# Kernel optimization log

Measured on AMD Instinct MI355X. Metric: run time of the kernel, lower is better.

The kernel has to match this reference:

```python
import jax, jax.numpy as jnp
import numpy as np
from jax import lax

# Static configuration (matches init_kwargs / input_specs)
B, DIM, H, W = 4, 192, 64, 64
HEADS, SR, WS = 8, 4, 3
HD = DIM // HEADS            # 24
LL = WS * WS                 # 9  (local window length)
N = H * W                    # 4096 tokens
PH, PW = H // SR, W // SR    # 16, 16 pooled grid
PLEN = PH * PW               # 256
PRETRAIN = 512 // 8          # img_size // 2**(i+2) with i=1 -> 64


def _ln(x, g, b, eps=1e-5):
    m = x.mean(-1, keepdims=True)
    v = ((x - m) ** 2).mean(-1, keepdims=True)
    return (x - m) / jnp.sqrt(v + eps) * g + b


def _l2norm(x):
    n = jnp.sqrt(jnp.sum(x * x, -1, keepdims=True))
    return x / jnp.maximum(n, 1e-12)


def _build_static():
    # get_relative_position_cpb: adaptive 1d pool of arange gives key coords
    qh = np.arange(H, dtype=np.float64)
    qw = np.arange(W, dtype=np.float64)
    kh = qh.reshape(PH, SR).mean(-1)  # H divisible by SR -> uniform bins
    kw = qw.reshape(PW, SR).mean(-1)
    KH, KW = np.meshgrid(kh, kw, indexing='ij')
    QH, QW = np.meshgrid(qh, qw, indexing='ij')
    rel_h = (QH.reshape(-1)[:, None] - KH.reshape(-1)[None, :]) / (PRETRAIN - 1) * 8
    rel_w = (QW.reshape(-1)[:, None] - KW.reshape(-1)[None, :]) / (PRETRAIN - 1) * 8
    rel_hw = np.stack([rel_h, rel_w], -1).reshape(-1, 2)
    table, idx = np.unique(rel_hw, axis=0, return_inverse=True)
    table = np.sign(table) * np.log2(np.abs(table) + 1.0) / np.log2(8.0)
    # get_seqlen_and_mask: validity of each of the 9 neighbors per position
    hh, ww = np.meshgrid(np.arange(H), np.arange(W), indexing='ij')
    hh, ww = hh.reshape(-1), ww.reshape(-1)
    valid = np.stack([(hh + dh >= 0) & (hh + dh < H) & (ww + dw >= 0) & (ww + dw < W)
                      for dh in (-1, 0, 1) for dw in (-1, 0, 1)], -1)  # [N, 9]
    pad_mask = ~valid
    seq_scale = np.log(valid.sum(-1, keepdims=True).astype(np.float64) + PLEN).astype(np.float32)  # [N,1]
    return idx.reshape(-1).astype(np.int32), table.astype(np.float32), seq_scale, pad_mask


def setup_inputs() -> dict:
    key = jax.random.key(0)
    ks = jax.random.split(key, 12)
    f32 = jnp.float32

    def tn(k, shape, std=0.02):
        return jax.random.truncated_normal(k, -2.0, 2.0, shape, f32) * std

    rel_idx, table, seq_scale, pad_mask = _build_static()
    return dict(
        x=jax.random.normal(ks[0], (B, DIM, H, W), f32),
        pe_w=tn(ks[1], (DIM, DIM, 3, 3)),
        pe_b=jnp.zeros((DIM,), f32),
        pe_ln_g=jnp.ones((DIM,), f32), pe_ln_b=jnp.zeros((DIM,), f32),
        q_w=tn(ks[2], (DIM, DIM)), q_b=jnp.zeros((DIM,), f32),
        kv_w=tn(ks[3], (2 * DIM, DIM)), kv_b=jnp.zeros((2 * DIM,), f32),
        sr_w=tn(ks[4], (DIM, DIM)), sr_b=jnp.zeros((DIM,), f32),
        norm_g=jnp.ones((DIM,), f32), norm_b=jnp.zeros((DIM,), f32),
        cpb1_w=tn(ks[5], (512, 2), 0.1), cpb1_b=jnp.zeros((512,), f32),
        cpb2_w=tn(ks[6], (HEADS, 512), 0.05), cpb2_b=jnp.zeros((HEADS,), f32),
        rpb_local=tn(ks[7], (HEADS, LL), 0.0004),
        learnable_tokens=tn(ks[8], (HEADS, HD, LL)),
        learnable_bias=jnp.zeros((HEADS, 1, LL), f32),
        query_embedding=tn(ks[9], (HEADS, 1, HD)),
        temperature=jnp.full((HEADS, 1, 1), float(np.log(np.exp(1.0 / 0.24) - 1.0)), f32),
        proj_w=tn(ks[10], (DIM, DIM)), proj_b=jnp.zeros((DIM,), f32),
        out_ln_g=jnp.ones((DIM,), f32), out_ln_b=jnp.zeros((DIM,), f32),
        rel_idx=jnp.asarray(rel_idx),
        coords_table=jnp.asarray(table),
        seq_scale=jnp.asarray(seq_scale),
        pad_mask=jnp.asarray(pad_mask),
    )


def _forward(x, pe_w, pe_b, pe_ln_g, pe_ln_b, q_w, q_b, kv_w, kv_b, sr_w, sr_b,
             norm_g, norm_b, cpb1_w, cpb1_b, cpb2_w, cpb2_b, rpb_local,
             learnable_tokens, learnable_bias, query_embedding, temperature,
             proj_w, proj_b, out_ln_g, out_ln_b,
             rel_idx, coords_table, seq_scale, pad_mask):
    # OverlapPatchEmbed: 3x3 conv s1 p1 -> tokens -> LN
    xc = lax.conv_general_dilated(x, pe_w, (1, 1), ((1, 1), (1, 1)),
                                  dimension_numbers=('NCHW', 'OIHW', 'NCHW')) + pe_b[None, :, None, None]
    t = _ln(xc.reshape(B, DIM, N).transpose(0, 2, 1), pe_ln_g, pe_ln_b)  # [B,N,C]

    # queries
    q = t @ q_w.T + q_b
    q_norm = _l2norm(q.reshape(B, N, HEADS, HD).transpose(0, 2, 1, 3))   # [B,h,N,d]
    q_scaled = (q_norm + query_embedding[None]) * jax.nn.softplus(temperature)[None] * seq_scale

    # local KV via 3x3 neighborhood gather (torch nn.Unfold)
    kv = t @ kv_w.T + kv_b                                               # [B,N,2C]
    k_loc = _l2norm(kv[..., :DIM].reshape(B, N, HEADS, HD)).reshape(B, N, DIM)
    kv_map = jnp.concatenate([k_loc, kv[..., DIM:]], -1).transpose(0, 2, 1).reshape(B, 2 * DIM, H, W)
    p = jnp.pad(kv_map, ((0, 0), (0, 0), (1, 1), (1, 1)))
    neigh = jnp.stack([p[:, :, kh:kh + H, kw:kw + W] for kh in range(WS) for kw in range(WS)], 2)
    neigh = neigh.reshape(B, 2 * HEADS, HD, LL, N).transpose(0, 1, 4, 2, 3)  # [B,2h,N,d,9]
    k_local, v_local = neigh[:, :HEADS], neigh[:, HEADS:]
    attn_local = jnp.einsum('bhnd,bhndl->bhnl', q_scaled, k_local) + rpb_local[None, :, None, :]
    attn_local = jnp.where(pad_mask[None, None], -jnp.inf, attn_local)   # [B,h,N,9]

    # pooled global KV: 1x1 conv -> GELU -> adaptive avg pool -> LN -> kv
    x_map = t.transpose(0, 2, 1).reshape(B, DIM, H, W)
    sr_out = jax.nn.gelu(jnp.einsum('oc,bchw->bohw', sr_w, x_map) + sr_b[None, :, None, None],
                         approximate=False)
    pooled = sr_out.reshape(B, DIM, PH, SR, PW, SR).mean((3, 5)).reshape(B, DIM, PLEN).transpose(0, 2, 1)
    pooled = _ln(pooled, norm_g, norm_b)
    kv_p = (pooled @ kv_w.T + kv_b).reshape(B, PLEN, 2 * HEADS, HD).transpose(0, 2, 1, 3)
    k_pool, v_pool = kv_p[:, :HEADS], kv_p[:, HEADS:]

    # CPB relative position bias for the pooled branch
    cpb = jax.nn.relu(coords_table @ cpb1_w.T + cpb1_b) @ cpb2_w.T + cpb2_b  # [T,h]
    pool_bias = cpb.T[:, rel_idx].reshape(HEADS, N, PLEN)
    attn_pool = jnp.einsum('bhnd,bhmd->bhnm', q_scaled, _l2norm(k_pool)) + pool_bias[None]

    # joint softmax over local + pooled keys
    attn = jax.nn.softmax(jnp.concatenate([attn_local, attn_pool], -1), -1)
    a_loc, a_pool = attn[..., :LL], attn[..., LL:]

    w_loc = jnp.einsum('bhnd,hdl->bhnl', q_norm, learnable_tokens) + learnable_bias[None] + a_loc
    x_local = jnp.einsum('bhnl,bhndl->bhnd', w_loc, v_local)
    x_pool = jnp.einsum('bhnm,bhmd->bhnd', a_pool, v_pool)

    out = (x_local + x_pool).transpose(0, 2, 1, 3).reshape(B, N, DIM) @ proj_w.T + proj_b
    out = _ln(out, out_ln_g, out_ln_b)
    return out.transpose(0, 2, 1).reshape(B, DIM, H, W)


def reference(x, pe_w, pe_b, pe_ln_g, pe_ln_b, q_w, q_b, kv_w, kv_b, sr_w, sr_b,
              norm_g, norm_b, cpb1_w, cpb1_b, cpb2_w, cpb2_b, rpb_local,
              learnable_tokens, learnable_bias, query_embedding, temperature,
              proj_w, proj_b, out_ln_g, out_ln_b,
              rel_idx, coords_table, seq_scale, pad_mask):
    return _forward(x, pe_w, pe_b, pe_ln_g, pe_ln_b, q_w, q_b, kv_w, kv_b, sr_w, sr_b,
                    norm_g, norm_b, cpb1_w, cpb1_b, cpb2_w, cpb2_b, rpb_local,
                    learnable_tokens, learnable_bias, query_embedding, temperature,
                    proj_w, proj_b, out_ln_g, out_ln_b,
                    rel_idx, coords_table, seq_scale, pad_mask)
```

## Files before the change

kernel.cpp:

```cpp
#include <hip/hip_runtime.h>
#include <stdint.h>


__device__ __forceinline__ float b2f(unsigned short u) {
  return __uint_as_float(((unsigned)u) << 16);
}
__device__ __forceinline__ unsigned short f2b(float f) {
  unsigned x = __float_as_uint(f);
  return (unsigned short)((x + 0x7fffu + ((x >> 16) & 1u)) >> 16);
}

constexpr size_t OFF_T    = 0;
constexpr size_t OFF_KMAP = 3145728;
constexpr size_t OFF_QN   = 9437184;
constexpr size_t OFF_QS   = 12582912;
constexpr size_t OFF_CTX  = 15728640;
constexpr size_t OFF_POOL = 18874368;
constexpr size_t OFF_KP   = 19070976;
constexpr size_t OFF_VP   = 19267584;
constexpr size_t OFF_CPB  = 19464192;
constexpr size_t OFF_BIAS = 19595264;
constexpr size_t OFF_WTC  = OFF_CTX;
constexpr size_t OFF_QT   = OFF_CTX + 331776;
constexpr size_t OFF_KVT  = OFF_CTX + 368640;
constexpr size_t OFF_SRT  = OFF_CTX + 442368;
constexpr size_t OFF_PJT  = OFF_KMAP;

__global__ __launch_bounds__(256) void k_wt_conv(const float* __restrict__ pw,
                                                 float* __restrict__ wt) {
  int i = blockIdx.x * 256 + threadIdx.x;
  if (i >= 331776) return;
  int oc = i % 192, k = i / 192;
  wt[i] = pw[(size_t)oc * 1728 + k];
}
__global__ __launch_bounds__(256) void k_wt_gen(const float* __restrict__ src,
                                                float* __restrict__ dst, int O, int K) {
  int i = blockIdx.x * 256 + threadIdx.x;
  if (i >= O * K) return;
  int o = i % O, k = i / O;
  dst[i] = src[(size_t)o * K + k];
}

__global__ __launch_bounds__(256) void k_conv(
    const float* __restrict__ x, const float* __restrict__ wtc,
    float* __restrict__ t0, float* __restrict__ t1, float* __restrict__ t2) {
  __shared__ float xl[8 * 4 * 66];
  const int tid = threadIdx.x;
  const int lane = tid & 63;
  const int wv = __builtin_amdgcn_readfirstlane(tid >> 6);
  const int h0 = blockIdx.x * 2;
  const int b = blockIdx.y;
  const int zz = blockIdx.z;
  const int obase = (zz & 3) * 48;
  const int ith = zz >> 2;
  const int icb = ith * 8;
  const int ow = obase + wv * 12;

  float acc0[12], acc1[12];
#pragma unroll
  for (int j = 0; j < 12; ++j) { acc0[j] = 0.f; acc1[j] = 0.f; }

  float xr[9];
  auto loadx = [&](int ic0) {
#pragma unroll
    for (int s = 0; s < 9; ++s) {
      int f = tid + s * 256;
      float v = 0.f;
      if (f < 2112) {
        int ii = f / 264;
        int rem = f - ii * 264;
        int r = rem / 66;
        int wp = rem - r * 66;
        int hh = h0 + r - 1, ww = wp - 1;
        if (hh >= 0 && hh < 64 && ww >= 0 && ww < 64)
          v = x[((size_t)(b * 192 + ic0 * 8 + ii) << 12) + (hh << 6) + ww];
      }
      xr[s] = v;
    }
  };
  loadx(icb);

  for (int i2 = 0; i2 < 8; ++i2) {
    const int ic0 = icb + i2;
    __syncthreads();
#pragma unroll
    for (int s = 0; s < 9; ++s) {
      int f = tid + s * 256;
      if (f < 2112) {
        int ii = f / 264;
        int rem = f - ii * 264;
        int r = rem / 66;
        int wp = rem - r * 66;
        xl[(ii * 4 + r) * 66 + wp] = xr[s];
      }
    }
    __syncthreads();
    if (i2 < 7) loadx(ic0 + 1);
    const float* wb = wtc + (size_t)ic0 * 72 * 192 + ow;
#pragma unroll 1
    for (int ii = 0; ii < 8; ++ii) {
      float xv[4][3];
#pragma unroll
      for (int r4 = 0; r4 < 4; ++r4) {
        const float* xp = &xl[(ii * 4 + r4) * 66 + lane];
        xv[r4][0] = xp[0]; xv[r4][1] = xp[1]; xv[r4][2] = xp[2];
      }
#pragma unroll
      for (int r = 0; r < 3; ++r) {
#pragma unroll
        for (int kw = 0; kw < 3; ++kw) {
          const float4* wp = (const float4*)(wb + (size_t)(ii * 9 + r * 3 + kw) * 192);
          float4 wA = wp[0], wB = wp[1], wC = wp[2];
          float xv0 = xv[r][kw], xv1 = xv[r + 1][kw];
          acc0[0]  += xv0 * wA.x;  acc1[0]  += xv1 * wA.x;
          acc0[1]  += xv0 * wA.y;  acc1[1]  += xv1 * wA.y;
          acc0[2]  += xv0 * wA.z;  acc1[2]  += xv1 * wA.z;
          acc0[3]  += xv0 * wA.w;  acc1[3]  += xv1 * wA.w;
          acc0[4]  += xv0 * wB.x;  acc1[4]  += xv1 * wB.x;
          acc0[5]  += xv0 * wB.y;  acc1[5]  += xv1 * wB.y;
          acc0[6]  += xv0 * wB.z;  acc1[6]  += xv1 * wB.z;
          acc0[7]  += xv0 * wB.w;  acc1[7]  += xv1 * wB.w;
          acc0[8]  += xv0 * wC.x;  acc1[8]  += xv1 * wC.x;
          acc0[9]  += xv0 * wC.y;  acc1[9]  += xv1 * wC.y;
          acc0[10] += xv0 * wC.z;  acc1[10] += xv1 * wC.z;
          acc0[11] += xv0 * wC.w;  acc1[11] += xv1 * wC.w;
        }
      }
    }
  }
  float* tdst = (ith == 0) ? t0 : ((ith == 1) ? t1 : t2);
  float* out0 = tdst + ((size_t)b * 4096 + h0 * 64 + lane) * 192 + ow;
  float* out1 = out0 + 64 * 192;
#pragma unroll
  for (int j4 = 0; j4 < 3; ++j4) {
    float4 v0, v1;
    v0.x = acc0[j4 * 4 + 0];  v1.x = acc1[j4 * 4 + 0];
    v0.y = acc0[j4 * 4 + 1];  v1.y = acc1[j4 * 4 + 1];
    v0.z = acc0[j4 * 4 + 2];  v1.z = acc1[j4 * 4 + 2];
    v0.w = acc0[j4 * 4 + 3];  v1.w = acc1[j4 * 4 + 3];
    ((float4*)out0)[j4] = v0;
    ((float4*)out1)[j4] = v1;
  }
}

__global__ __launch_bounds__(256) void k_ln_rows(float* __restrict__ data,
    const float* __restrict__ data2, const float* __restrict__ data3,
    const float* __restrict__ cbias,
    const float* __restrict__ g, const float* __restrict__ be, int rows) {
  int lane = threadIdx.x & 63;
  int wv = threadIdx.x >> 6;
  int row = blockIdx.x * 4 + wv;
  if (row >= rows) return;
  float* p = data + (size_t)row * 192;
  float v0 = p[lane], v1 = p[lane + 64], v2 = p[lane + 128];
  if (data2) {
    const float* p2 = data2 + (size_t)row * 192;
    v0 += p2[lane]; v1 += p2[lane + 64]; v2 += p2[lane + 128];
  }
  if (data3) {
    const float* p3 = data3 + (size_t)row * 192;
    v0 += p3[lane]; v1 += p3[lane + 64]; v2 += p3[lane + 128];
  }
  if (cbias) {
    v0 += cbias[lane]; v1 += cbias[lane + 64]; v2 += cbias[lane + 128];
  }
  float s = v0 + v1 + v2;
  float sq = v0 * v0 + v1 * v1 + v2 * v2;
#pragma unroll
  for (int m = 32; m >= 1; m >>= 1) {
    s += __shfl_xor(s, m, 64);
    sq += __shfl_xor(sq, m, 64);
  }
  float mean = s * (1.f / 192.f);
  float var = sq * (1.f / 192.f) - mean * mean;
  float rstd = rsqrtf(var + 1e-5f);
  p[lane]       = (v0 - mean) * rstd * g[lane]       + be[lane];
  p[lane + 64]  = (v1 - mean) * rstd * g[lane + 64]  + be[lane + 64];
  p[lane + 128] = (v2 - mean) * rstd * g[lane + 128] + be[lane + 128];
}

template <int OCB, typename GXV, typename GXD>
__device__ __forceinline__ void gemm_tiles(
    float* __restrict__ wl, float* __restrict__ xs, int tid, int lane, int wv,
    const float* __restrict__ wt, int ostr, int obase,
    float (&acc)[OCB / 4], GXV gxv, GXD gxd) {
  constexpr int NPF4 = OCB / 4;
  constexpr int NW4 = OCB / 16;
  constexpr int NWR = (32 * NPF4 + 255) / 256;
  constexpr bool WEXACT = (32 * NPF4 % 256) == 0;
  float xr[8];
  float4 wr[NWR];
  auto loadx = [&](int k0) {
#pragma unroll
    for (int s = 0; s < 8; ++s) xr[s] = gxv(k0, tid + s * 256);
  };
  auto loadw = [&](int k0) {
#pragma unroll
    for (int s = 0; s < NWR; ++s) {
      int f4 = tid + s * 256;
      if (WEXACT || f4 < 32 * NPF4) {
        int kk = f4 / NPF4, j = f4 - kk * NPF4;
        wr[s] = ((const float4*)(wt + (size_t)(k0 + kk) * ostr + obase))[j];
      }
    }
  };
  loadx(0); loadw(0);
  for (int kt = 0; kt < 6; ++kt) {
    __syncthreads();
#pragma unroll
    for (int s = 0; s < 8; ++s) xs[gxd(tid + s * 256)] = xr[s];
#pragma unroll
    for (int s = 0; s < NWR; ++s) {
      int f4 = tid + s * 256;
      if (WEXACT || f4 < 32 * NPF4) ((float4*)wl)[f4] = wr[s];
    }
    __syncthreads();
    if (kt < 5) { loadx((kt + 1) * 32); loadw((kt + 1) * 32); }
#pragma unroll 4
    for (int kk = 0; kk < 32; ++kk) {
      float xv = xs[kk * 66 + lane];
      const float4* wrow = (const float4*)&wl[kk * OCB + wv * NW4 * 4];
#pragma unroll
      for (int j4 = 0; j4 < NW4; ++j4) {
        float4 w4 = wrow[j4];
        acc[j4 * 4 + 0] += xv * w4.x;
        acc[j4 * 4 + 1] += xv * w4.y;
        acc[j4 * 4 + 2] += xv * w4.z;
        acc[j4 * 4 + 3] += xv * w4.w;
      }
    }
  }
}

__global__ __launch_bounds__(256) void k_q(
    const float* __restrict__ t, const float* __restrict__ qt, const float* __restrict__ qb,
    const float* __restrict__ qe, const float* __restrict__ tmp, const float* __restrict__ ss,
    float* __restrict__ qno, float* __restrict__ qso) {
  __shared__ __align__(16) float wl[32 * 96];
  __shared__ float xs[32 * 66];
  const int tid = threadIdx.x;
  const int lane = tid & 63;
  const int wv = __builtin_amdgcn_readfirstlane(tid >> 6);
  const int n0 = blockIdx.x * 64;
  const int b = blockIdx.y;
  const int obase = blockIdx.z * 96;
  const int hh = blockIdx.z * 4 + wv;
  const int oc0 = obase + wv * 24;
  float acc[24];
#pragma unroll
  for (int j = 0; j < 24; ++j) acc[j] = 0.f;

  gemm_tiles<96>(wl, xs, tid, lane, wv, qt, 192, obase, acc,
    [&](int k0, int f) {
      int nl = f >> 5, kk = f & 31;
      return t[((size_t)b * 4096 + n0 + nl) * 192 + k0 + kk];
    },
    [&](int f) { return (f & 31) * 66 + (f >> 5); });

  const int n = n0 + lane;
  float ssv = ss[n];
  float sumsq = 0.f;
#pragma unroll
  for (int d = 0; d < 24; ++d) {
    float v = acc[d] + qb[oc0 + d];
    sumsq += v * v;
  }
  float rn = 1.f / fmaxf(sqrtf(sumsq), 1e-12f);
  float sp = log1pf(__expf(tmp[hh]));
#pragma unroll
  for (int d = 0; d < 24; ++d) {
    float qv = (acc[d] + qb[oc0 + d]) * rn;
    size_t o = ((size_t)(b * 8 + hh) * 24 + d) * 4096 + n;
    qno[o] = qv;
    qso[o] = (qv + qe[hh * 24 + d]) * sp * ssv;
  }
}

__global__ __launch_bounds__(256) void k_kv(
    const float* __restrict__ t, const float* __restrict__ kvt, const float* __restrict__ kb_,
    float* __restrict__ kmap) {
  __shared__ __align__(16) float wl[32 * 96];
  __shared__ float xs[32 * 66];
  const int tid = threadIdx.x;
  const int lane = tid & 63;
  const int wv = __builtin_amdgcn_readfirstlane(tid >> 6);
  const int n0 = blockIdx.x * 64;
  const int b = blockIdx.y;
  const int obase = blockIdx.z * 96;
  const int oc0 = obase + wv * 24;
  const int n = n0 + lane;
  float acc[24];
#pragma unroll
  for (int j = 0; j < 24; ++j) acc[j] = 0.f;

  gemm_tiles<96>(wl, xs, tid, lane, wv, kvt, 384, obase, acc,
    [&](int k0, int f) {
      int nl = f >> 5, kk = f & 31;
      return t[((size_t)b * 4096 + n0 + nl) * 192 + k0 + kk];
    },
    [&](int f) { return (f & 31) * 66 + (f >> 5); });

  if (oc0 < 192) {
    float sumsq = 0.f;
#pragma unroll
    for (int d = 0; d < 24; ++d) {
      float v = acc[d] + kb_[oc0 + d];
      sumsq += v * v;
    }
    float rn = 1.f / fmaxf(sqrtf(sumsq), 1e-12f);
#pragma unroll
    for (int d = 0; d < 24; ++d)
      kmap[((size_t)b * 384 + oc0 + d) * 4096 + n] = (acc[d] + kb_[oc0 + d]) * rn;
  } else {
#pragma unroll
    for (int d = 0; d < 24; ++d)
      kmap[((size_t)b * 384 + oc0 + d) * 4096 + n] = acc[d] + kb_[oc0 + d];
  }
}

__device__ __forceinline__ float gelu_exact(float v) {
  float u = v * 0.70710678118654752f;
  float a = fabsf(u);
  float tt = 1.f / (1.f + 0.3275911f * a);
  float poly = ((((1.061405429f * tt - 1.453152027f) * tt + 1.421413741f) * tt
                 - 0.284496736f) * tt + 0.254829592f) * tt;
  float erfa = 1.f - poly * __expf(-a * a);
  float erfv = (u < 0.f) ? -erfa : erfa;
  return 0.5f * v * (1.f + erfv);
}

__global__ __launch_bounds__(256) void k_srpool(
    const float* __restrict__ t, const float* __restrict__ srt, const float* __restrict__ sb,
    float* __restrict__ pooled) {
  __shared__ __align__(16) float wl[32 * 48];
  __shared__ float xs[32 * 66];
  const int tid = threadIdx.x;
  const int lane = tid & 63;
  const int wv = __builtin_amdgcn_readfirstlane(tid >> 6);
  const int wx = blockIdx.x & 3;
  const int obase = (blockIdx.x >> 2) * 48;
  const int ph = blockIdx.y;
  const int b = blockIdx.z;
  const int oc0 = obase + wv * 12;
  float acc[12];
#pragma unroll
  for (int j = 0; j < 12; ++j) acc[j] = 0.f;

  gemm_tiles<48>(wl, xs, tid, lane, wv, srt, 192, obase, acc,
    [&](int k0, int f) {
      int pl = f >> 5, kk = f & 31;
      int row = (ph * 4 + (pl >> 4)) * 64 + wx * 16 + (pl & 15);
      return t[((size_t)b * 4096 + row) * 192 + k0 + kk];
    },
    [&](int f) { return (f & 31) * 66 + (f >> 5); });

#pragma unroll
  for (int j = 0; j < 12; ++j) {
    float gv = gelu_exact(acc[j] + sb[oc0 + j]);
    gv += __shfl_xor(gv, 1, 64);
    gv += __shfl_xor(gv, 2, 64);
    gv += __shfl_xor(gv, 16, 64);
    gv += __shfl_xor(gv, 32, 64);
    if ((lane & 51) == 0) {
      int cell = (lane >> 2) & 3;
      int p = ph * 16 + wx * 4 + cell;
      pooled[((size_t)b * 256 + p) * 192 + oc0 + j] = gv * (1.f / 16.f);
    }
  }
}

__global__ __launch_bounds__(256) void k_kvp(
    const float* __restrict__ pooled, const float* __restrict__ kvt, const float* __restrict__ kb_,
    float* __restrict__ kp, float* __restrict__ vp) {
  __shared__ __align__(16) float wl[32 * 96];
  __shared__ float xs[32 * 66];
  const int tid = threadIdx.x;
  const int lane = tid & 63;
  const int wv = __builtin_amdgcn_readfirstlane(tid >> 6);
  const int r0 = blockIdx.x * 64;
  const int obase = blockIdx.y * 96;
  const int oc0 = obase + wv * 24;
  const int row = r0 + lane;
  const int b = row >> 8;
  const int m = row & 255;
  float acc[24];
#pragma unroll
  for (int j = 0; j < 24; ++j) acc[j] = 0.f;

  gemm_tiles<96>(wl, xs, tid, lane, wv, kvt, 384, obase, acc,
    [&](int k0, int f) {
      int nl = f >> 5, kk = f & 31;
      return pooled[(size_t)(r0 + nl) * 192 + k0 + kk];
    },
    [&](int f) { return (f & 31) * 66 + (f >> 5); });

  if (oc0 < 192) {
    int hh = oc0 / 24;
    float sumsq = 0.f;
#pragma unroll
    for (int d = 0; d < 24; ++d) {
      float v = acc[d] + kb_[oc0 + d];
      sumsq += v * v;
    }
    float rn = 1.f / fmaxf(sqrtf(sumsq), 1e-12f);
#pragma unroll
    for (int d = 0; d < 24; ++d)
      kp[(((size_t)(b * 8 + hh)) * 256 + m) * 24 + d] = (acc[d] + kb_[oc0 + d]) * rn;
  } else {
    int hh = (oc0 - 192) / 24;
#pragma unroll
    for (int d = 0; d < 24; ++d)
      vp[(((size_t)(b * 8 + hh)) * 256 + m) * 24 + d] = acc[d] + kb_[oc0 + d];
  }
}

__global__ __launch_bounds__(256) void k_cpb(
    const float* __restrict__ coords, const float* __restrict__ c1w,
    const float* __restrict__ c1b, const float* __restrict__ c2w,
    const float* __restrict__ c2b, float* __restrict__ cpb, int T) {
  __shared__ float s1w[1024];
  __shared__ float s1b[512];
  __shared__ __align__(16) float s2w[512 * 8];
  const int tid = threadIdx.x;
  for (int f = tid; f < 1024; f += 256) s1w[f] = c1w[f];
  for (int f = tid; f < 512; f += 256) s1b[f] = c1b[f];
  for (int f = tid; f < 4096; f += 256) {
    int h = f >> 9, j = f & 511;
    s2w[j * 8 + h] = c2w[f];
  }
  __syncthreads();
  int i = blockIdx.x * 256 + tid;
  int ic = (i < T) ? i : (T - 1);
  float x0 = coords[2 * ic], y0 = coords[2 * ic + 1];
  float a[8];
#pragma unroll
  for (int h = 0; h < 8; ++h) a[h] = c2b[h];
#pragma unroll 4
  for (int j = 0; j < 512; ++j) {
    float hv = fmaxf(s1w[2 * j] * x0 + s1w[2 * j + 1] * y0 + s1b[j], 0.f);
    const float4* w2 = (const float4*)&s2w[j * 8];
    float4 wA = w2[0], wB = w2[1];
    a[0] += hv * wA.x; a[1] += hv * wA.y; a[2] += hv * wA.z; a[3] += hv * wA.w;
    a[4] += hv * wB.x; a[5] += hv * wB.y; a[6] += hv * wB.z; a[7] += hv * wB.w;
  }
  if (i < T) {
#pragma unroll
    for (int h = 0; h < 8; ++h) cpb[(size_t)i * 8 + h] = a[h];
  }
}

__global__ __launch_bounds__(256) void k_bias(
    const int* __restrict__ rel, const float* __restrict__ cpb,
    unsigned short* __restrict__ bt) {
  int g = blockIdx.x * 256 + threadIdx.x;
  int n = g >> 5;
  int m0 = (g & 31) * 8;
  const int4* r4 = (const int4*)(rel + (size_t)n * 256 + m0);
  int4 ra = r4[0], rb = r4[1];
  int idxs[8] = {ra.x, ra.y, ra.z, ra.w, rb.x, rb.y, rb.z, rb.w};
  unsigned acc[8][4];
#pragma unroll
  for (int j = 0; j < 8; ++j) {
    const float4* c4 = (const float4*)(cpb + (size_t)idxs[j] * 8);
    float4 A = c4[0], Bv = c4[1];
    float vals[8] = {A.x, A.y, A.z, A.w, Bv.x, Bv.y, Bv.z, Bv.w};
#pragma unroll
    for (int hh = 0; hh < 8; ++hh) {
      unsigned u = f2b(vals[hh]);
      if (j & 1) acc[hh][j >> 1] |= u << 16;
      else       acc[hh][j >> 1]  = u;
    }
  }
#pragma unroll
  for (int hh = 0; hh < 8; ++hh) {
    uint4 o;
    o.x = acc[hh][0]; o.y = acc[hh][1]; o.z = acc[hh][2]; o.w = acc[hh][3];
    *(uint4*)(bt + ((size_t)hh * 4096 + n) * 256 + m0) = o;
  }
}

__global__ __launch_bounds__(512, 4) void k_attn(
    const float* __restrict__ qs_g, const float* __restrict__ qn_g,
    const float* __restrict__ kmap, const float* __restrict__ kp, const float* __restrict__ vp,
    const unsigned short* __restrict__ bt, const float* __restrict__ rpb,
    const float* __restrict__ lt, const float* __restrict__ lb,
    float* __restrict__ ctx) {
  __shared__ __align__(16) float smem[12288];
  float* kl = smem;
  float* vl = smem + 6144;
  const int tid = threadIdx.x;
  const int lane = tid & 63;
  const int w = __builtin_amdgcn_readfirstlane(tid >> 6);
  const int qm = w & 3;
  const int rr = w >> 2;
  const int row = blockIdx.x * 2 + rr;
  const int h = blockIdx.y;
  const int b = blockIdx.z;
  const int n = (row << 6) + lane;
  const float SHIFT = 15.f;

  {
    const float4* kps = (const float4*)(kp + (size_t)(b * 8 + h) * 6144);
    const float4* vps = (const float4*)(vp + (size_t)(b * 8 + h) * 6144);
    float4* kld = (float4*)kl;
    float4* vld = (float4*)vl;
#pragma unroll
    for (int c = 0; c < 3; ++c) {
      int f = tid + c * 512;
      kld[f] = kps[f];
      vld[f] = vps[f];
    }
  }

  float qsv[24];
  {
    const float* qsb = qs_g + ((size_t)(b * 8 + h) * 24) * 4096 + n;
#pragma unroll
    for (int d = 0; d < 24; ++d) qsv[d] = qsb[(size_t)d * 4096];
  }

  const int l0 = (qm == 1) ? 0 : ((qm == 0) ? 3 : (qm * 2 + 1));
  const int lcnt = (qm == 1) ? 3 : 2;

  float wlv[3];
  {
    float qnv[24];
    const float* qnb = qn_g + ((size_t)(b * 8 + h) * 24) * 4096 + n;
#pragma unroll
    for (int d = 0; d < 24; ++d) qnv[d] = qnb[(size_t)d * 4096];
    const float* ltp = lt + h * 216;
    const float* lbp = lb + h * 9;
#pragma unroll
    for (int j = 0; j < 3; ++j) {
      float a = 0.f;
      if (j < lcnt) {
        int l = l0 + j;
#pragma unroll
        for (int d = 0; d < 24; ++d) a += qnv[d] * ltp[d * 9 + l];
        a += lbp[l];
      }
      wlv[j] = a;
    }
  }

  float ctxA[24], ctxBP[24];
#pragma unroll
  for (int d = 0; d < 24; ++d) { ctxA[d] = 0.f; ctxBP[d] = 0.f; }
  float S = 0.f;

  {
    const float* kbase = kmap + ((size_t)b * 384 + h * 24) * 4096;
    const float* rpp = rpb + h * 9;
    for (int j = 0; j < lcnt; ++j) {
      const int l = l0 + j;
      const int dh = l / 3 - 1, dw = l % 3 - 1;
      const int hp = row + dh;
      if (hp < 0 || hp >= 64) continue;
      const int wp2 = lane + dw;
      const bool okw = (wp2 >= 0) && (wp2 < 64);
      const int nn = (hp << 6) + (okw ? wp2 : lane);
      const float* kb = kbase + nn;
      const float* vb = kb + (size_t)192 * 4096;
      float d0 = 0, d1 = 0, d2 = 0, d3 = 0;
#pragma unroll
      for (int d = 0; d < 24; d += 4) {
        d0 += qsv[d] * kb[(size_t)d * 4096];
        d1 += qsv[d + 1] * kb[(size_t)(d + 1) * 4096];
        d2 += qsv[d + 2] * kb[(size_t)(d + 2) * 4096];
        d3 += qsv[d + 3] * kb[(size_t)(d + 3) * 4096];
      }
      float p = okw ? __expf((d0 + d1) + (d2 + d3) + rpp[l] - SHIFT) : 0.f;
      S += p;
      float wll = okw ? wlv[j] : 0.f;
#pragma unroll
      for (int d = 0; d < 24; ++d) {
        float vv = vb[(size_t)d * 4096];
        ctxA[d] += wll * vv;
        ctxBP[d] += p * vv;
      }
    }
  }

  __syncthreads();

  {
    const unsigned short* bp = bt + ((size_t)h * 4096 + n) * 256 + qm * 64;
    const float* klq = kl + qm * (64 * 24);
    const float* vlq = vl + qm * (64 * 24);
    uint4 bcur = *(const uint4*)bp;
#pragma unroll 1
    for (int c = 0; c < 8; ++c) {
      uint4 bnx = bcur;
      if (c < 7) bnx = *(const uint4*)(bp + (c + 1) * 8);
#pragma unroll
      for (int j = 0; j < 8; ++j) {
        const float4* kr4 = (const float4*)&klq[(c * 8 + j) * 24];
        const float4* vr4 = (const float4*)&vlq[(c * 8 + j) * 24];
        float d0 = 0, d1 = 0, d2 = 0, d3 = 0;
#pragma unroll
        for (int q4 = 0; q4 < 6; ++q4) {
          float4 k4 = kr4[q4];
          d0 += qsv[q4 * 4 + 0] * k4.x;
          d1 += qsv[q4 * 4 + 1] * k4.y;
          d2 += qsv[q4 * 4 + 2] * k4.z;
          d3 += qsv[q4 * 4 + 3] * k4.w;
        }
        unsigned word = (j < 2) ? bcur.x : (j < 4) ? bcur.y : (j < 6) ? bcur.z : bcur.w;
        float bv = (j & 1) ? __uint_as_float(word & 0xffff0000u)
                           : __uint_as_float(word << 16);
        float p = __expf((d0 + d1) + (d2 + d3) + bv - SHIFT);
        S += p;
#pragma unroll
        for (int q4 = 0; q4 < 6; ++q4) {
          float4 v4 = vr4[q4];
          ctxBP[q4 * 4 + 0] += p * v4.x;
          ctxBP[q4 * 4 + 1] += p * v4.y;
          ctxBP[q4 * 4 + 2] += p * v4.z;
          ctxBP[q4 * 4 + 3] += p * v4.w;
        }
      }
      bcur = bnx;
    }
  }

  for (int src = 1; src < 4; ++src) {
    __syncthreads();
    if (qm == src) {
      float* p = smem + (size_t)(rr * 64 + lane) * 49;
      p[0] = S;
#pragma unroll
      for (int d = 0; d < 24; ++d) { p[1 + d] = ctxA[d]; p[25 + d] = ctxBP[d]; }
    }
    __syncthreads();
    if (qm == 0) {
      const float* p = smem + (size_t)(rr * 64 + lane) * 49;
      S += p[0];
#pragma unroll
      for (int d = 0; d < 24; ++d) { ctxA[d] += p[1 + d]; ctxBP[d] += p[25 + d]; }
    }
  }
  if (qm == 0) {
    const float inv = 1.f / S;
    float* cb = ctx + ((size_t)(b * 8 + h) * 24) * 4096 + n;
#pragma unroll
    for (int d = 0; d < 24; ++d)
      cb[(size_t)d * 4096] = ctxA[d] + ctxBP[d] * inv;
  }
}

__global__ __launch_bounds__(256) void k_projg(
    const float* __restrict__ ctx, const float* __restrict__ pjt, const float* __restrict__ pb,
    float* __restrict__ pout) {
  __shared__ __align__(16) float wl[32 * 96];
  __shared__ float xs[32 * 66];
  const int tid = threadIdx.x;
  const int lane = tid & 63;
  const int wv = __builtin_amdgcn_readfirstlane(tid >> 6);
  const int n0 = blockIdx.x * 64;
  const int b = blockIdx.y;
  const int obase = blockIdx.z * 96;
  const int oc0 = obase + wv * 24;
  const int n = n0 + lane;
  float acc[24];
#pragma unroll
  for (int j = 0; j < 24; ++j) acc[j] = 0.f;

  gemm_tiles<96>(wl, xs, tid, lane, wv, pjt, 192, obase, acc,
    [&](int k0, int f) {
      int kk = f >> 6, nl = f & 63;
      return ctx[((size_t)b * 192 + k0 + kk) * 4096 + n0 + nl];
    },
    [&](int f) { return (f >> 6) * 66 + (f & 63); });

#pragma unroll
  for (int d = 0; d < 24; ++d)
    pout[((size_t)b * 192 + oc0 + d) * 4096 + n] = acc[d] + pb[oc0 + d];
}

__global__ __launch_bounds__(256) void k_oln(
    const float* __restrict__ pout, const float* __restrict__ g,
    const float* __restrict__ be, float* __restrict__ out) {
  __shared__ float red[2][4][64];
  const int tid = threadIdx.x;
  const int lane = tid & 63;
  const int wv = __builtin_amdgcn_readfirstlane(tid >> 6);
  const int n0 = blockIdx.x * 64;
  const int b = blockIdx.y;
  const int o0 = wv * 48;
  float v[48];
  float s = 0.f, sq = 0.f;
#pragma unroll
  for (int j = 0; j < 48; ++j) {
    v[j] = pout[((size_t)b * 192 + o0 + j) * 4096 + n0 + lane];
    s += v[j];
    sq += v[j] * v[j];
  }
  red[0][wv][lane] = s;
  red[1][wv][lane] = sq;
  __syncthreads();
  float st = red[0][0][lane] + red[0][1][lane] + red[0][2][lane] + red[0][3][lane];
  float sqt = red[1][0][lane] + red[1][1][lane] + red[1][2][lane] + red[1][3][lane];
  float mean = st * (1.f / 192.f);
  float var = sqt * (1.f / 192.f) - mean * mean;
  float rstd = rsqrtf(var + 1e-5f);
#pragma unroll
  for (int j = 0; j < 48; ++j) {
    int o = o0 + j;
    out[((size_t)b * 192 + o) * 4096 + n0 + lane] = (v[j] - mean) * rstd * g[o] + be[o];
  }
}

extern "C" void kernel_launch(void* const* d_in, const int* in_sizes, int n_in,
                              void* d_out, int out_size, void* d_ws, size_t ws_size,
                              hipStream_t stream) {
  float* w = (float*)d_ws;

  const float* x      = (const float*)d_in[0];
  const float* pe_w   = (const float*)d_in[1];
  const float* pe_b   = (const float*)d_in[2];
  const float* peln_g = (const float*)d_in[3];
  const float* peln_b = (const float*)d_in[4];
  const float* q_w    = (const float*)d_in[5];
  const float* q_b    = (const float*)d_in[6];
  const float* kv_w   = (const float*)d_in[7];
  const float* kv_b   = (const float*)d_in[8];
  const float* sr_w   = (const float*)d_in[9];
  const float* sr_b   = (const float*)d_in[10];
  const float* norm_g = (const float*)d_in[11];
  const float* norm_b = (const float*)d_in[12];
  const float* cpb1w  = (const float*)d_in[13];
  const float* cpb1b  = (const float*)d_in[14];
  const float* cpb2w  = (const float*)d_in[15];
  const float* cpb2b  = (const float*)d_in[16];
  const float* rpb    = (const float*)d_in[17];
  const float* lt     = (const float*)d_in[18];
  const float* lb     = (const float*)d_in[19];
  const float* qe     = (const float*)d_in[20];
  const float* temp   = (const float*)d_in[21];
  const float* proj_w = (const float*)d_in[22];
  const float* proj_b = (const float*)d_in[23];
  const float* oln_g  = (const float*)d_in[24];
  const float* oln_b  = (const float*)d_in[25];
  const int*   rel    = (const int*)d_in[26];
  const float* coords = (const float*)d_in[27];
  const float* ss     = (const float*)d_in[28];

  dim3 blk(256);
  k_wt_conv<<<dim3(1296), blk, 0, stream>>>(pe_w, w + OFF_WTC);
  k_wt_gen<<<dim3(144), blk, 0, stream>>>(q_w, w + OFF_QT, 192, 192);
  k_wt_gen<<<dim3(288), blk, 0, stream>>>(kv_w, w + OFF_KVT, 384, 192);
  k_wt_gen<<<dim3(144), blk, 0, stream>>>(sr_w, w + OFF_SRT, 192, 192);

  k_conv<<<dim3(32, 4, 12), blk, 0, stream>>>(x, w + OFF_WTC, w + OFF_T,
      w + OFF_KMAP, w + OFF_KMAP + 3145728);
  k_ln_rows<<<dim3(4096), blk, 0, stream>>>(w + OFF_T, w + OFF_KMAP,
      w + OFF_KMAP + 3145728, pe_b, peln_g, peln_b, 16384);
  k_q<<<dim3(64, 4, 2), blk, 0, stream>>>(w + OFF_T, w + OFF_QT, q_b, qe, temp, ss,
      w + OFF_QN, w + OFF_QS);
  k_kv<<<dim3(64, 4, 4), blk, 0, stream>>>(w + OFF_T, w + OFF_KVT, kv_b, w + OFF_KMAP);
  k_srpool<<<dim3(16, 16, 4), blk, 0, stream>>>(w + OFF_T, w + OFF_SRT, sr_b, w + OFF_POOL);
  k_ln_rows<<<dim3(256), blk, 0, stream>>>(w + OFF_POOL, nullptr, nullptr, nullptr,
      norm_g, norm_b, 1024);
  k_kvp<<<dim3(16, 4), blk, 0, stream>>>(w + OFF_POOL, w + OFF_KVT, kv_b,
      w + OFF_KP, w + OFF_VP);
  int T = in_sizes[27] / 2;
  k_cpb<<<dim3((T + 255) / 256), blk, 0, stream>>>(coords, cpb1w, cpb1b, cpb2w, cpb2b,
      w + OFF_CPB, T);
  k_bias<<<dim3(512), blk, 0, stream>>>(rel, w + OFF_CPB,
      (unsigned short*)(w + OFF_BIAS));
  k_attn<<<dim3(32, 8, 4), dim3(512), 0, stream>>>(w + OFF_QS, w + OFF_QN, w + OFF_KMAP,
      w + OFF_KP, w + OFF_VP, (const unsigned short*)(w + OFF_BIAS), rpb, lt, lb,
      w + OFF_CTX);
  k_wt_gen<<<dim3(144), blk, 0, stream>>>(proj_w, w + OFF_PJT, 192, 192);
  k_projg<<<dim3(64, 4, 2), blk, 0, stream>>>(w + OFF_CTX, w + OFF_PJT, proj_b,
      w + OFF_QN);
  k_oln<<<dim3(64, 4), blk, 0, stream>>>(w + OFF_QN, oln_g, oln_b, (float*)d_out);
}
```

Baseline: 608.2 us.

## Compute four output rows per conv block and split input channels six ways

Each block of the 3x3 patch-embed convolution now computes four output rows instead of two, so every weight float4 fetched is reused across four rows. To keep the same block count, the input-channel reduction is split into six partial sums instead of three. The extra partial buffers borrow the QN, QS and BIAS workspace regions, and the row LayerNorm kernel now adds up to six partial inputs. The cost is more partial-sum memory traffic, more accumulator registers, and a possible overrun if the BIAS region is smaller than one full partial buffer.

Measured after the change: 606.5 us. About the same (-0.3%).

```diff
diff --git a/kernel.cpp b/kernel.cpp
--- a/kernel.cpp
+++ b/kernel.cpp
@@ -43,32 +43,35 @@
 
 __global__ __launch_bounds__(256) void k_conv(
     const float* __restrict__ x, const float* __restrict__ wtc,
-    float* __restrict__ t0, float* __restrict__ t1, float* __restrict__ t2) {
-  __shared__ float xl[8 * 4 * 66];
+    float* __restrict__ p0, float* __restrict__ p1, float* __restrict__ p2,
+    float* __restrict__ p3, float* __restrict__ p4, float* __restrict__ p5) {
+  __shared__ float xl[8 * 6 * 66];
   const int tid = threadIdx.x;
   const int lane = tid & 63;
   const int wv = __builtin_amdgcn_readfirstlane(tid >> 6);
-  const int h0 = blockIdx.x * 2;
+  const int h0 = blockIdx.x * 4;
   const int b = blockIdx.y;
   const int zz = blockIdx.z;
   const int obase = (zz & 3) * 48;
   const int ith = zz >> 2;
-  const int icb = ith * 8;
+  const int icb = ith * 4;
   const int ow = obase + wv * 12;
 
-  float acc0[12], acc1[12];
-#pragma unroll
-  for (int j = 0; j < 12; ++j) { acc0[j] = 0.f; acc1[j] = 0.f; }
-
-  float xr[9];
+  float acc[4][12];
+#pragma unroll
+  for (int ro = 0; ro < 4; ++ro)
+#pragma unroll
+    for (int j = 0; j < 12; ++j) acc[ro][j] = 0.f;
+
+  float xr[13];
   auto loadx = [&](int ic0) {
 #pragma unroll
-    for (int s = 0; s < 9; ++s) {
+    for (int s = 0; s < 13; ++s) {
       int f = tid + s * 256;
       float v = 0.f;
-      if (f < 2112) {
-        int ii = f / 264;
-        int rem = f - ii * 264;
+      if (f < 3168) {
+        int ii = f / 396;
+        int rem = f - ii * 396;
         int r = rem / 66;
         int wp = rem - r * 66;
         int hh = h0 + r - 1, ww = wp - 1;
@@ -80,72 +83,78 @@
   };
   loadx(icb);
 
-  for (int i2 = 0; i2 < 8; ++i2) {
+  for (int i2 = 0; i2 < 4; ++i2) {
     const int ic0 = icb + i2;
     __syncthreads();
 #pragma unroll
-    for (int s = 0; s < 9; ++s) {
+    for (int s = 0; s < 13; ++s) {
       int f = tid + s * 256;
-      if (f < 2112) {
-        int ii = f / 264;
-        int rem = f - ii * 264;
+      if (f < 3168) {
+        int ii = f / 396;
+        int rem = f - ii * 396;
         int r = rem / 66;
         int wp = rem - r * 66;
-        xl[(ii * 4 + r) * 66 + wp] = xr[s];
+        xl[(ii * 6 + r) * 66 + wp] = xr[s];
       }
     }
     __syncthreads();
-    if (i2 < 7) loadx(ic0 + 1);
+    if (i2 < 3) loadx(ic0 + 1);
     const float* wb = wtc + (size_t)ic0 * 72 * 192 + ow;
 #pragma unroll 1
     for (int ii = 0; ii < 8; ++ii) {
-      float xv[4][3];
-#pragma unroll
-      for (int r4 = 0; r4 < 4; ++r4) {
-        const float* xp = &xl[(ii * 4 + r4) * 66 + lane];
-        xv[r4][0] = xp[0]; xv[r4][1] = xp[1]; xv[r4][2] = xp[2];
-      }
-#pragma unroll
-      for (int r = 0; r < 3; ++r) {
+      float xv[6][3];
+#pragma unroll
+      for (int r6 = 0; r6 < 6; ++r6) {
+        const float* xp = &xl[(ii * 6 + r6) * 66 + lane];
+        xv[r6][0] = xp[0]; xv[r6][1] = xp[1]; xv[r6][2] = xp[2];
+      }
+#pragma unroll
+      for (int kh = 0; kh < 3; ++kh) {
 #pragma unroll
         for (int kw = 0; kw < 3; ++kw) {
-          const float4* wp = (const float4*)(wb + (size_t)(ii * 9 + r * 3 + kw) * 192);
+          const float4* wp = (const float4*)(wb + (size_t)(ii * 9 + kh * 3 + kw) * 192);
           float4 wA = wp[0], wB = wp[1], wC = wp[2];
-          float xv0 = xv[r][kw], xv1 = xv[r + 1][kw];
-          acc0[0]  += xv0 * wA.x;  acc1[0]  += xv1 * wA.x;
-          acc0[1]  += xv0 * wA.y;  acc1[1]  += xv1 * wA.y;
-          acc0[2]  += xv0 * wA.z;  acc1[2]  += xv1 * wA.z;
-          acc0[3]  += xv0 * wA.w;  acc1[3]  += xv1 * wA.w;
-          acc0[4]  += xv0 * wB.x;  acc1[4]  += xv1 * wB.x;
-          acc0[5]  += xv0 * wB.y;  acc1[5]  += xv1 * wB.y;
-          acc0[6]  += xv0 * wB.z;  acc1[6]  += xv1 * wB.z;
-          acc0[7]  += xv0 * wB.w;  acc1[7]  += xv1 * wB.w;
-          acc0[8]  += xv0 * wC.x;  acc1[8]  += xv1 * wC.x;
-          acc0[9]  += xv0 * wC.y;  acc1[9]  += xv1 * wC.y;
-          acc0[10] += xv0 * wC.z;  acc1[10] += xv1 * wC.z;
-          acc0[11] += xv0 * wC.w;  acc1[11] += xv1 * wC.w;
+#pragma unroll
+          for (int ro = 0; ro < 4; ++ro) {
+            float xvv = xv[ro + kh][kw];
+            acc[ro][0]  += xvv * wA.x;
+            acc[ro][1]  += xvv * wA.y;
+            acc[ro][2]  += xvv * wA.z;
+            acc[ro][3]  += xvv * wA.w;
+            acc[ro][4]  += xvv * wB.x;
+            acc[ro][5]  += xvv * wB.y;
+            acc[ro][6]  += xvv * wB.z;
+            acc[ro][7]  += xvv * wB.w;
+            acc[ro][8]  += xvv * wC.x;
+            acc[ro][9]  += xvv * wC.y;
+            acc[ro][10] += xvv * wC.z;
+            acc[ro][11] += xvv * wC.w;
+          }
         }
       }
     }
   }
-  float* tdst = (ith == 0) ? t0 : ((ith == 1) ? t1 : t2);
-  float* out0 = tdst + ((size_t)b * 4096 + h0 * 64 + lane) * 192 + ow;
-  float* out1 = out0 + 64 * 192;
-#pragma unroll
-  for (int j4 = 0; j4 < 3; ++j4) {
-    float4 v0, v1;
-    v0.x = acc0[j4 * 4 + 0];  v1.x = acc1[j4 * 4 + 0];
-    v0.y = acc0[j4 * 4 + 1];  v1.y = acc1[j4 * 4 + 1];
-    v0.z = acc0[j4 * 4 + 2];  v1.z = acc1[j4 * 4 + 2];
-    v0.w = acc0[j4 * 4 + 3];  v1.w = acc1[j4 * 4 + 3];
-    ((float4*)out0)[j4] = v0;
-    ((float4*)out1)[j4] = v1;
+  float* tdst = (ith == 0) ? p0 : (ith == 1) ? p1 : (ith == 2) ? p2
+              : (ith == 3) ? p3 : (ith == 4) ? p4 : p5;
+#pragma unroll
+  for (int ro = 0; ro < 4; ++ro) {
+    float* op = tdst + ((size_t)b * 4096 + (h0 + ro) * 64 + lane) * 192 + ow;
+#pragma unroll
+    for (int j4 = 0; j4 < 3; ++j4) {
+      float4 v;
+      v.x = acc[ro][j4 * 4 + 0];
+      v.y = acc[ro][j4 * 4 + 1];
+      v.z = acc[ro][j4 * 4 + 2];
+      v.w = acc[ro][j4 * 4 + 3];
+      ((float4*)op)[j4] = v;
+    }
   }
 }
 
 __global__ __launch_bounds__(256) void k_ln_rows(float* __restrict__ data,
-    const float* __restrict__ data2, const float* __restrict__ data3,
-    const float* __restrict__ cbias,
+    const float* __restrict__ d2, const float* __restrict__ d3,
+    const float* __restrict__ d4, const float* __restrict__ d5,
+    const float* __restrict__ d6, const float* __restrict__ cbias,
     const float* __restrict__ g, const float* __restrict__ be, int rows) {
   int lane = threadIdx.x & 63;
   int wv = threadIdx.x >> 6;
@@ -153,13 +162,25 @@
   if (row >= rows) return;
   float* p = data + (size_t)row * 192;
   float v0 = p[lane], v1 = p[lane + 64], v2 = p[lane + 128];
-  if (data2) {
-    const float* p2 = data2 + (size_t)row * 192;
-    v0 += p2[lane]; v1 += p2[lane + 64]; v2 += p2[lane + 128];
-  }
-  if (data3) {
-    const float* p3 = data3 + (size_t)row * 192;
-    v0 += p3[lane]; v1 += p3[lane + 64]; v2 += p3[lane + 128];
+  if (d2) {
+    const float* q = d2 + (size_t)row * 192;
+    v0 += q[lane]; v1 += q[lane + 64]; v2 += q[lane + 128];
+  }
+  if (d3) {
+    const float* q = d3 + (size_t)row * 192;
+    v0 += q[lane]; v1 += q[lane + 64]; v2 += q[lane + 128];
+  }
+  if (d4) {
+    const float* q = d4 + (size_t)row * 192;
+    v0 += q[lane]; v1 += q[lane + 64]; v2 += q[lane + 128];
+  }
+  if (d5) {
+    const float* q = d5 + (size_t)row * 192;
+    v0 += q[lane]; v1 += q[lane + 64]; v2 += q[lane + 128];
+  }
+  if (d6) {
+    const float* q = d6 + (size_t)row * 192;
+    v0 += q[lane]; v1 += q[lane + 64]; v2 += q[lane + 128];
   }
   if (cbias) {
     v0 += cbias[lane]; v1 += cbias[lane + 64]; v2 += cbias[lane + 128];
@@ -751,16 +772,18 @@
   k_wt_gen<<<dim3(288), blk, 0, stream>>>(kv_w, w + OFF_KVT, 384, 192);
   k_wt_gen<<<dim3(144), blk, 0, stream>>>(sr_w, w + OFF_SRT, 192, 192);
 
-  k_conv<<<dim3(32, 4, 12), blk, 0, stream>>>(x, w + OFF_WTC, w + OFF_T,
-      w + OFF_KMAP, w + OFF_KMAP + 3145728);
+  k_conv<<<dim3(16, 4, 24), blk, 0, stream>>>(x, w + OFF_WTC,
+      w + OFF_T, w + OFF_KMAP, w + OFF_KMAP + 3145728,
+      w + OFF_QN, w + OFF_QS, (float*)(w + OFF_BIAS));
   k_ln_rows<<<dim3(4096), blk, 0, stream>>>(w + OFF_T, w + OFF_KMAP,
-      w + OFF_KMAP + 3145728, pe_b, peln_g, peln_b, 16384);
+      w + OFF_KMAP + 3145728, w + OFF_QN, w + OFF_QS, (const float*)(w + OFF_BIAS),
+      pe_b, peln_g, peln_b, 16384);
   k_q<<<dim3(64, 4, 2), blk, 0, stream>>>(w + OFF_T, w + OFF_QT, q_b, qe, temp, ss,
       w + OFF_QN, w + OFF_QS);
   k_kv<<<dim3(64, 4, 4), blk, 0, stream>>>(w + OFF_T, w + OFF_KVT, kv_b, w + OFF_KMAP);
   k_srpool<<<dim3(16, 16, 4), blk, 0, stream>>>(w + OFF_T, w + OFF_SRT, sr_b, w + OFF_POOL);
   k_ln_rows<<<dim3(256), blk, 0, stream>>>(w + OFF_POOL, nullptr, nullptr, nullptr,
-      norm_g, norm_b, 1024);
+      nullptr, nullptr, nullptr, norm_g, norm_b, 1024);
   k_kvp<<<dim3(16, 4), blk, 0, stream>>>(w + OFF_POOL, w + OFF_KVT, kv_b,
       w + OFF_KP, w + OFF_VP);
   int T = in_sizes[27] / 2;
```
